# Performance work log

Hardware: AMD Instinct MI355X
Metric: run time of the kernel (lower is better)

## Reference

```python
import jax, jax.numpy as jnp
import numpy as np

N, E, D, F, H = 20000, 600000, 128, 128, 4
C = 2 * D + F  # concat(source, sink, edge) feature dim


def _ln(x, g, b, eps=1e-5):
    mu = jnp.mean(x, -1, keepdims=True)
    v = jnp.mean((x - mu) ** 2, -1, keepdims=True)
    return (x - mu) / jnp.sqrt(v + eps) * g + b


def _gelu(x):
    return jax.nn.gelu(x, approximate=False)  # torch default exact GELU


def setup_inputs() -> dict:
    key = jax.random.key(0)
    ks = iter(jax.random.split(key, 40))

    def nrm(shape, s=0.05):
        return jax.random.normal(next(ks), shape, dtype=jnp.float32) * s

    inp = {}
    inp["bb_nodes"] = jax.random.normal(next(ks), (N, D), dtype=jnp.float32)
    inp["eattr"] = jax.random.normal(next(ks), (E, F), dtype=jnp.float32)
    inp["eidx"] = jax.random.randint(next(ks), (2, E), 0, N)
    inp["aW_w"] = nrm((H, D, C)); inp["aW_b"] = nrm((H, D))
    inp["aA_w"] = nrm((H, D));    inp["aA_b"] = nrm((H,))
    inp["nw1"] = nrm((D, C)); inp["nb1"] = nrm((D,))
    inp["nw2"] = nrm((D, D)); inp["nb2"] = nrm((D,))
    inp["nw3"] = nrm((D, D)); inp["nb3"] = nrm((D,))
    inp["dw1"] = nrm((4 * D, D)); inp["db1"] = nrm((4 * D,))
    inp["dw2"] = nrm((D, 4 * D)); inp["db2"] = nrm((D,))
    inp["ew1"] = nrm((F, C)); inp["eb1"] = nrm((F,))
    inp["ew2"] = nrm((F, F)); inp["eb2"] = nrm((F,))
    inp["ew3"] = nrm((F, F)); inp["eb3"] = nrm((F,))
    inp["aggr_w"] = nrm((D, H * D)); inp["aggr_b"] = nrm((D,))
    inp["ln1_g"] = jnp.ones((D,), jnp.float32); inp["ln1_b"] = jnp.zeros((D,), jnp.float32)
    inp["lne_g"] = jnp.ones((F,), jnp.float32); inp["lne_b"] = jnp.zeros((F,), jnp.float32)
    return inp


def reference(bb_nodes, eattr, eidx, aW_w, aW_b, aA_w, aA_b,
              nw1, nb1, nw2, nb2, nw3, nb3,
              dw1, db1, dw2, db2,
              ew1, eb1, ew2, eb2, ew3, eb3,
              aggr_w, aggr_b, ln1_g, ln1_b, lne_g, lne_b):
    n = bb_nodes.shape[0]
    src, snk = eidx[0], eidx[1]
    h = jnp.concatenate([bb_nodes[src], bb_nodes[snk], eattr], axis=1)  # [E, 2D+F]
    nheads = aW_w.shape[0]
    # per-head GAT-style logits; loop over small fixed head count to keep
    # peak memory at [E, D] per head rather than [H, E, D]
    logits = jnp.stack(
        [jax.nn.leaky_relu(h @ aW_w[k].T + aW_b[k], 0.2) @ aA_w[k] + aA_b[k]
         for k in range(nheads)], axis=1)                              # [E, H]
    msg = _gelu(h @ nw1.T + nb1)
    msg = _gelu(msg @ nw2.T + nb2)
    msg = msg @ nw3.T + nb3                                            # [E, D]
    # segment softmax over incoming edges of each sink node
    smax = jax.ops.segment_max(logits, snk, num_segments=n)            # [N, H]
    att = jnp.exp(logits - smax[snk])                                  # [E, H]
    norm = jax.ops.segment_sum(att + 1e-12, snk, num_segments=n)       # [N, H]
    att = att / norm[snk]
    # NOTE: faithful to the original's `atten[:, eidx[1]]` which re-gathers
    # the per-EDGE attention along the edge axis using NODE indices.
    att_g = att[snk]                                                   # [E, H]
    agg = jnp.stack(
        [jax.ops.segment_sum(att_g[:, k, None] * msg, snk, num_segments=n)
         for k in range(nheads)], axis=1)                              # [N, H, D]
    upd = agg.reshape(n, -1) @ aggr_w.T + aggr_b                       # [N, D]
    x = _ln(bb_nodes + upd, ln1_g, ln1_b)
    dense = _gelu(x @ dw1.T + db1) @ dw2.T + db2
    # original adds the attention update (not x) in the second residual,
    # and reuses node_norm1 both times (node_norm2 is dead code)
    x = _ln(dense + upd, ln1_g, ln1_b)
    eu = jnp.concatenate([x[src], x[snk], eattr], axis=1)              # [E, 2D+F]
    eu = _gelu(eu @ ew1.T + eb1)
    eu = _gelu(eu @ ew2.T + eb2)
    eu = eu @ ew3.T + eb3
    eout = _ln(eattr + eu, lne_g, lne_b)
    return x, eout
```

## Files before the change

### kernel.cpp

```cpp
#include <hip/hip_runtime.h>
#include <hip/hip_bf16.h>

#define N_NODES 20000
#define N_EDGES 600000
#define HEADS 4
#define MAXDEG 128

#define WOFF_AW   0
#define WOFF_NW1  196608
#define WOFF_NW2  245760
#define WOFF_NW3  262144
#define WOFF_EW1  278528
#define WOFF_EW2  327680
#define WOFF_EW3  344064
#define WOFF_AG   360448
#define WOFF_DW1  425984
#define WOFF_DW2  491520
#define WPACK_TOT 557056

typedef __attribute__((ext_vector_type(8))) short s16x8;
typedef __attribute__((ext_vector_type(4))) float f32x4;
typedef unsigned int u32;
typedef unsigned short u16;

__device__ __forceinline__ float bf2f(u16 h){ return __uint_as_float(((u32)h)<<16); }
__device__ __forceinline__ u16 f2bf(float f){
  u32 u = __float_as_uint(f) + 0x8000u;
  return (u16)(u>>16);
}
__device__ __forceinline__ float gelu_f(float x){
  float z2 = 1.5957691216057308f*(x + 0.044715f*x*x*x);
  float e = __expf(z2);
  float th = 1.f - 2.f/(e + 1.f);
  return 0.5f*x*(1.f + th);
}

__device__ __forceinline__ int swzf(int row){ return (row&15)<<4; }

__global__ __launch_bounds__(256) void k_pack(
    const float* __restrict__ aW, const float* __restrict__ nw1, const float* __restrict__ nw2,
    const float* __restrict__ nw3, const float* __restrict__ ew1, const float* __restrict__ ew2,
    const float* __restrict__ ew3, const float* __restrict__ aggr_w, const float* __restrict__ dw1,
    const float* __restrict__ dw2, const float* __restrict__ bb,
    u16* __restrict__ wpk, u16* __restrict__ bbp)
{
  int i = blockIdx.x*256 + threadIdx.x;
  if (i < WPACK_TOT){
    const float* src; int rel; int KROW;
    if      (i < WOFF_NW1){ src=aW;     rel=i;           KROW=384; }
    else if (i < WOFF_NW2){ src=nw1;    rel=i-WOFF_NW1;  KROW=384; }
    else if (i < WOFF_NW3){ src=nw2;    rel=i-WOFF_NW2;  KROW=128; }
    else if (i < WOFF_EW1){ src=nw3;    rel=i-WOFF_NW3;  KROW=128; }
    else if (i < WOFF_EW2){ src=ew1;    rel=i-WOFF_EW1;  KROW=384; }
    else if (i < WOFF_EW3){ src=ew2;    rel=i-WOFF_EW2;  KROW=128; }
    else if (i < WOFF_AG) { src=ew3;    rel=i-WOFF_EW3;  KROW=128; }
    else if (i < WOFF_DW1){ src=aggr_w; rel=i-WOFF_AG;   KROW=512; }
    else if (i < WOFF_DW2){ src=dw1;    rel=i-WOFF_DW1;  KROW=128; }
    else                  { src=dw2;    rel=i-WOFF_DW2;  KROW=512; }
    int e = rel&7, lane = (rel>>3)&63, frag = rel>>9;
    int ks, g;
    if      (KROW==384){ ks = frag % 12; g = frag / 12; }
    else if (KROW==128){ ks = frag & 3;  g = frag >> 2; }
    else               { ks = frag & 15; g = frag >> 4; }
    int row = g*16 + (lane&15);
    int k   = ks*32 + ((lane>>4)&3)*8 + e;
    wpk[i] = f2bf(src[(size_t)row*KROW + k]);
  }
  if (i < N_NODES*128) bbp[i] = f2bf(bb[i]);
}

__global__ __launch_bounds__(256) void k_init(float* __restrict__ norm, u32* __restrict__ cnt)
{
  int i = blockIdx.x*256 + threadIdx.x;
  if (i < N_NODES*HEADS) norm[i] = 0.f;
  if (i < N_NODES) cnt[i] = 0u;
}

template<int NT, int KS, int RS>
__device__ __forceinline__ void gemmF(const char* ab, const u16* __restrict__ wfrag,
                                      int g0, int l, f32x4 (&acc)[4][NT])
{
  const int l15 = l&15, lg = l>>4;
  const int swz = l15<<4;
  const u16* wl = wfrag + l*8;
  #pragma unroll 4
  for (int ks=0; ks<KS; ++ks){
    s16x8 af[4];
    #pragma unroll
    for (int mt=0;mt<4;++mt)
      af[mt] = *(const s16x8*)(ab + (mt*16+l15)*RS + (((ks*4+lg)*16) ^ swz));
    #pragma unroll
    for (int nt=0;nt<NT;++nt){
      s16x8 bf = *(const s16x8*)(wl + (size_t)((g0+nt)*KS + ks)*512);
      #pragma unroll
      for (int mt=0;mt<4;++mt)
        acc[mt][nt] = __builtin_amdgcn_mfma_f32_16x16x32_bf16(af[mt], bf, acc[mt][nt], 0,0,0);
    }
  }
}

template<int KSI, int RS, int KSTOT>
__device__ __forceinline__ void gemmF2(const char* ab, const u16* __restrict__ wfrag,
                                       int g0, int ks0, int l, f32x4 (&acc)[4][1])
{
  const int l15 = l&15, lg = l>>4;
  const int swz = l15<<4;
  const u16* wl = wfrag + l*8;
  #pragma unroll 4
  for (int ks=0; ks<KSI; ++ks){
    s16x8 af[4];
    #pragma unroll
    for (int mt=0;mt<4;++mt)
      af[mt] = *(const s16x8*)(ab + (mt*16+l15)*RS + (((ks*4+lg)*16) ^ swz));
    s16x8 bf = *(const s16x8*)(wl + (size_t)(g0*KSTOT + ks0 + ks)*512);
    #pragma unroll
    for (int mt=0;mt<4;++mt)
      acc[mt][0] = __builtin_amdgcn_mfma_f32_16x16x32_bf16(af[mt], bf, acc[mt][0], 0,0,0);
  }
}

template<int RS>
__device__ __forceinline__ void writeReg(char* hsb, int regionByte, int col, int lg,
                                         const float (&v)[4][4])
{
  #pragma unroll
  for (int mt=0;mt<4;++mt){
    #pragma unroll
    for (int r=0;r<4;++r){
      int row = mt*16 + lg*4 + r;
      *(u16*)(hsb + row*RS + regionByte + ((col*2) ^ swzf(row))) = f2bf(v[mt][r]);
    }
  }
}

__device__ __forceinline__ void stage512(char* hsb, const u16* __restrict__ ntab,
                                         const float* __restrict__ eattr, const int* __restrict__ eidx,
                                         int e0, int t)
{
  const int row = t>>3, p = t&7, ge = e0+row;
  const int swz = swzf(row);
  char* rp = hsb + row*768;
  if (p < 4){
    int nid = eidx[(p<2 ? 0 : N_EDGES) + ge];
    const int4* srow = (const int4*)(ntab + (size_t)nid*128);
    const int base = (p<2) ? 0 : 16;
    #pragma unroll
    for (int s=0;s<8;++s){
      int ci = (2*s + p) & 15;
      int4 v = srow[ci];
      *(int4*)(rp + (((base+ci)*16) ^ swz)) = v;
    }
  } else {
    int q = p-4;
    const float* er = eattr + (size_t)ge*128 + q*32;
    #pragma unroll
    for (int c=0;c<4;++c){
      float4 x0 = ((const float4*)er)[c*2];
      float4 x1 = ((const float4*)er)[c*2+1];
      int4 v;
      v.x = (int)((u32)f2bf(x0.x) | ((u32)f2bf(x0.y)<<16));
      v.y = (int)((u32)f2bf(x0.z) | ((u32)f2bf(x0.w)<<16));
      v.z = (int)((u32)f2bf(x1.x) | ((u32)f2bf(x1.y)<<16));
      v.w = (int)((u32)f2bf(x1.z) | ((u32)f2bf(x1.w)<<16));
      *(int4*)(rp + (((32 + q*4 + c)*16) ^ swz)) = v;
    }
  }
}

__global__ __launch_bounds__(512,4) void k_edgeA(
  const u16* __restrict__ bbp, const float* __restrict__ eattr, const int* __restrict__ eidx,
  const u16* __restrict__ wpk,
  const float* __restrict__ aW_b, const float* __restrict__ aA_w, const float* __restrict__ aA_b,
  const float* __restrict__ nb1, const float* __restrict__ nb2, const float* __restrict__ nb3,
  float* __restrict__ logits, float* __restrict__ norm, u32* __restrict__ cnt,
  int* __restrict__ eids2, u16* __restrict__ msg)
{
  __shared__ u16 hs[64*384];
  __shared__ float lpart[8*64];
  __shared__ int snkid[64];
  char* hsb = (char*)hs;
  const int t = threadIdx.x;
  const int e0 = blockIdx.x*64;
  const int w = t>>6, l = t&63, l15 = l&15, lg = l>>4;
  const int col = w*16 + l15;

  stage512(hsb, bbp, eattr, eidx, e0, t);
  lpart[w*64 + l] = 0.f;
  if (t < 64){
    int k = eidx[N_EDGES + e0 + t];
    snkid[t] = k;
    u32 pos = atomicAdd(&cnt[k], 1u);
    if (pos < MAXDEG) eids2[k*MAXDEG + pos] = e0 + t;
  }
  __syncthreads();

  {
    #pragma unroll
    for (int ch=0; ch<2; ++ch){
      f32x4 acc[4][2];
      #pragma unroll
      for (int mt=0;mt<4;++mt){
        #pragma unroll
        for (int nt=0;nt<2;++nt){ f32x4 z={0.f,0.f,0.f,0.f}; acc[mt][nt]=z; }
      }
      int g0 = (w>>1)*8 + (w&1)*4 + ch*2;
      gemmF<2,12,768>(hsb, wpk+WOFF_AW, g0, l, acc);
      float lp[4][4];
      #pragma unroll
      for (int a=0;a<4;++a){
        #pragma unroll
        for (int b=0;b<4;++b) lp[a][b]=0.f;
      }
      #pragma unroll
      for (int nt=0;nt<2;++nt){
        int gcol = (w>>1)*128 + (w&1)*64 + ch*32 + nt*16 + l15;
        float bia = aW_b[gcol];
        float avw = aA_w[gcol];
        #pragma unroll
        for (int mt=0;mt<4;++mt){
          #pragma unroll
          for (int r=0;r<4;++r){
            float T = acc[mt][nt][r] + bia;
            T = (T>0.f) ? T : 0.2f*T;
            lp[mt][r] += T*avw;
          }
        }
      }
      #pragma unroll
      for (int mt=0;mt<4;++mt){
        #pragma unroll
        for (int r=0;r<4;++r){
          float v = lp[mt][r];
          v += __shfl_xor(v,1);
          v += __shfl_xor(v,2);
          v += __shfl_xor(v,4);
          v += __shfl_xor(v,8);
          if (l15==0) lpart[w*64 + mt*16 + lg*4 + r] += v;
        }
      }
    }
  }
  float m1v[4][4];
  {
    f32x4 acc[4][1];
    #pragma unroll
    for (int mt=0;mt<4;++mt){ f32x4 z={0.f,0.f,0.f,0.f}; acc[mt][0]=z; }
    gemmF<1,12,768>(hsb, wpk+WOFF_NW1, w, l, acc);
    float b = nb1[col];
    #pragma unroll
    for (int mt=0;mt<4;++mt){
      #pragma unroll
      for (int r=0;r<4;++r) m1v[mt][r] = gelu_f(acc[mt][0][r] + b);
    }
  }
  __syncthreads();

  if (t < 256){
    int row = t>>2, h = t&3;
    float s = lpart[(2*h)*64 + row] + lpart[(2*h+1)*64 + row] + aA_b[h];
    int e = e0 + row;
    logits[e*HEADS + h] = s;
    atomicAdd(&norm[snkid[row]*HEADS + h], expf(s));
  }
  writeReg<768>(hsb, 0, col, lg, m1v);
  __syncthreads();

  {
    f32x4 acc[4][1];
    #pragma unroll
    for (int mt=0;mt<4;++mt){ f32x4 z={0.f,0.f,0.f,0.f}; acc[mt][0]=z; }
    gemmF<1,4,768>(hsb, wpk+WOFF_NW2, w, l, acc);
    float b = nb2[col];
    float v[4][4];
    #pragma unroll
    for (int mt=0;mt<4;++mt){
      #pragma unroll
      for (int r=0;r<4;++r) v[mt][r] = gelu_f(acc[mt][0][r] + b);
    }
    writeReg<768>(hsb, 256, col, lg, v);
  }
  __syncthreads();

  {
    f32x4 acc[4][1];
    #pragma unroll
    for (int mt=0;mt<4;++mt){ f32x4 z={0.f,0.f,0.f,0.f}; acc[mt][0]=z; }
    gemmF<1,4,768>(hsb+256, wpk+WOFF_NW3, w, l, acc);
    float b = nb3[col];
    float v[4][4];
    #pragma unroll
    for (int mt=0;mt<4;++mt){
      #pragma unroll
      for (int r=0;r<4;++r) v[mt][r] = acc[mt][0][r] + b;
    }
    writeReg<768>(hsb, 512, col, lg, v);
  }
  __syncthreads();

  {
    int row = t>>3, p = t&7;
    const int swz = swzf(row);
    #pragma unroll
    for (int c=0;c<2;++c){
      int j = c*8 + p;
      int4 v = *(const int4*)(hsb + row*768 + 512 + ((j*16) ^ swz));
      *(int4*)((char*)msg + (size_t)(e0+row)*256 + j*16) = v;
    }
  }
}

__global__ __launch_bounds__(256) void k_msgsumZ(
  const u16* __restrict__ msg, const int* __restrict__ eids2, const u32* __restrict__ cnt,
  const int* __restrict__ eidx, const float* __restrict__ logits,
  const float* __restrict__ norm,
  u16* __restrict__ z)
{
  __shared__ float red[4][128];
  __shared__ float av[4];
  const int n = blockIdx.x, t = threadIdx.x;
  u32* zrow = (u32*)z + (size_t)n*256;
  if (n >= N_NODES){
    zrow[t] = 0u;
    return;
  }
  const int w = t>>6, l = t&63;
  int ecnt = (int)cnt[n]; if (ecnt > MAXDEG) ecnt = MAXDEG;
  float a0=0.f, a1=0.f;
  for (int i=w; i<ecnt; i+=4){
    int e = eids2[n*MAXDEG + i];
    u32 v = *(const u32*)(msg + (size_t)e*128 + l*2);
    a0 += __uint_as_float(v<<16);
    a1 += __uint_as_float(v & 0xFFFF0000u);
  }
  red[w][l*2] = a0; red[w][l*2+1] = a1;
  if (t < 4){
    int sn = eidx[N_EDGES + n];
    float c = 1e-12f * (float)cnt[sn];
    av[t] = expf(logits[n*HEADS+t]) / (norm[sn*HEADS+t] + c);
  }
  __syncthreads();
  int h = t>>6, dp = (t&63)*2;
  float s0 = red[0][dp]+red[1][dp]+red[2][dp]+red[3][dp];
  float s1 = red[0][dp+1]+red[1][dp+1]+red[2][dp+1]+red[3][dp+1];
  float a = av[h];
  zrow[h*64 + (t&63)] = (u32)f2bf(a*s0) | ((u32)f2bf(a*s1)<<16);
}

__global__ __launch_bounds__(512,2) void k_node(
  const u16* __restrict__ z, const float* __restrict__ bb,
  const u16* __restrict__ wpk, const float* __restrict__ aggr_b,
  const float* __restrict__ db1, const float* __restrict__ db2,
  const float* __restrict__ lng, const float* __restrict__ lnb,
  float* __restrict__ xout, u16* __restrict__ xbp)
{
  __shared__ u16 hs[64*512];
  __shared__ float lps[8*64];
  __shared__ float lpss[8*64];
  __shared__ float mrs[2*64];
  char* hsb = (char*)hs;
  const int t = threadIdx.x;
  const int nbase = blockIdx.x*64;
  const int w = t>>6, l = t&63, l15 = l&15, lg = l>>4;
  const int col = w*16 + l15;

  {
    const int row = t>>3, p = t&7;
    const int swz = swzf(row);
    char* rp = hsb + row*1024;
    const int4* zr = (const int4*)((const char*)z + (size_t)(nbase+row)*1024);
    #pragma unroll
    for (int c=0;c<8;++c){
      int ci = c*8 + p;
      int4 v = zr[ci];
      *(int4*)(rp + ((ci*16) ^ swz)) = v;
    }
  }
  __syncthreads();

  float v[4][4];
  {
    f32x4 acc[4][1];
    #pragma unroll
    for (int mt=0;mt<4;++mt){ f32x4 z_={0.f,0.f,0.f,0.f}; acc[mt][0]=z_; }
    gemmF<1,16,1024>(hsb, wpk+WOFF_AG, w, l, acc);
    float ab = aggr_b[col];
    #pragma unroll
    for (int mt=0;mt<4;++mt){
      #pragma unroll
      for (int r=0;r<4;++r) v[mt][r] = acc[mt][0][r] + ab;
    }
  }
  __syncthreads();

  {
    float xv[4][4];
    #pragma unroll
    for (int mt=0;mt<4;++mt){
      #pragma unroll
      for (int r=0;r<4;++r){
        int row = mt*16 + lg*4 + r;
        int ge = nbase + row; if (ge >= N_NODES) ge = N_NODES-1;
        xv[mt][r] = bb[(size_t)ge*128 + col] + v[mt][r];
      }
    }
    #pragma unroll
    for (int mt=0;mt<4;++mt){
      #pragma unroll
      for (int r=0;r<4;++r){
        float a = xv[mt][r], b = xv[mt][r]*xv[mt][r];
        a += __shfl_xor(a,1); b += __shfl_xor(b,1);
        a += __shfl_xor(a,2); b += __shfl_xor(b,2);
        a += __shfl_xor(a,4); b += __shfl_xor(b,4);
        a += __shfl_xor(a,8); b += __shfl_xor(b,8);
        if (l15==0){
          int row = mt*16 + lg*4 + r;
          lps[w*64 + row] = a;
          lpss[w*64 + row] = b;
        }
      }
    }
    __syncthreads();
    if (t < 64){
      float a=0.f, b=0.f;
      #pragma unroll
      for (int j=0;j<8;++j){ a += lps[j*64+t]; b += lpss[j*64+t]; }
      float mu = a*(1.f/128.f);
      float var = b*(1.f/128.f) - mu*mu;
      mrs[t] = mu;
      mrs[64+t] = rsqrtf(var + 1e-5f);
    }
    __syncthreads();
    float g = lng[col], bt = lnb[col];
    float xb[4][4];
    #pragma unroll
    for (int mt=0;mt<4;++mt){
      #pragma unroll
      for (int r=0;r<4;++r){
        int row = mt*16 + lg*4 + r;
        xb[mt][r] = (xv[mt][r] - mrs[row])*mrs[64+row]*g + bt;
      }
    }
    writeReg<1024>(hsb, 0, col, lg, xb);
  }
  __syncthreads();

  f32x4 acc3[4][1];
  #pragma unroll
  for (int mt=0;mt<4;++mt){ f32x4 z_={0.f,0.f,0.f,0.f}; acc3[mt][0]=z_; }
  #pragma unroll
  for (int c=0;c<4;++c){
    {
      f32x4 acc[4][1];
      #pragma unroll
      for (int mt=0;mt<4;++mt){ f32x4 z_={0.f,0.f,0.f,0.f}; acc[mt][0]=z_; }
      gemmF<1,4,1024>(hsb, wpk+WOFF_DW1, c*8 + w, l, acc);
      float b1 = db1[c*128 + col];
      float dh[4][4];
      #pragma unroll
      for (int mt=0;mt<4;++mt){
        #pragma unroll
        for (int r=0;r<4;++r) dh[mt][r] = gelu_f(acc[mt][0][r] + b1);
      }
      writeReg<1024>(hsb, 256 + (c&1)*256, col, lg, dh);
    }
    __syncthreads();
    gemmF2<4,1024,16>(hsb + 256 + (c&1)*256, wpk+WOFF_DW2, w, c*4, l, acc3);
  }

  {
    float ov[4][4];
    float b2 = db2[col];
    #pragma unroll
    for (int mt=0;mt<4;++mt){
      #pragma unroll
      for (int r=0;r<4;++r) ov[mt][r] = acc3[mt][0][r] + b2 + v[mt][r];
    }
    #pragma unroll
    for (int mt=0;mt<4;++mt){
      #pragma unroll
      for (int r=0;r<4;++r){
        float a = ov[mt][r], b = ov[mt][r]*ov[mt][r];
        a += __shfl_xor(a,1); b += __shfl_xor(b,1);
        a += __shfl_xor(a,2); b += __shfl_xor(b,2);
        a += __shfl_xor(a,4); b += __shfl_xor(b,4);
        a += __shfl_xor(a,8); b += __shfl_xor(b,8);
        if (l15==0){
          int row = mt*16 + lg*4 + r;
          lps[w*64 + row] = a;
          lpss[w*64 + row] = b;
        }
      }
    }
    __syncthreads();
    if (t < 64){
      float a=0.f, b=0.f;
      #pragma unroll
      for (int j=0;j<8;++j){ a += lps[j*64+t]; b += lpss[j*64+t]; }
      float mu = a*(1.f/128.f);
      float var = b*(1.f/128.f) - mu*mu;
      mrs[t] = mu;
      mrs[64+t] = rsqrtf(var + 1e-5f);
    }
    __syncthreads();
    float g = lng[col], bt = lnb[col];
    #pragma unroll
    for (int mt=0;mt<4;++mt){
      #pragma unroll
      for (int r=0;r<4;++r){
        int row = mt*16 + lg*4 + r;
        int ge = nbase + row;
        if (ge < N_NODES){
          float o = (ov[mt][r] - mrs[row])*mrs[64+row]*g + bt;
          xout[(size_t)ge*128 + col] = o;
          xbp[(size_t)ge*128 + col] = f2bf(o);
        }
      }
    }
  }
}

__global__ __launch_bounds__(512,4) void k_edgeC(
  const u16* __restrict__ xbp, const float* __restrict__ eattr, const int* __restrict__ eidx,
  const u16* __restrict__ wpk,
  const float* __restrict__ eb1, const float* __restrict__ eb2, const float* __restrict__ eb3,
  const float* __restrict__ lng, const float* __restrict__ lnb,
  float* __restrict__ eout)
{
  __shared__ u16 hs[64*384];
  __shared__ float wps[8*64];
  __shared__ float wpss[8*64];
  __shared__ float mrs[2*64];
  char* hsb=(char*)hs;
  const int t = threadIdx.x;
  const int e0 = blockIdx.x*64;
  const int w = t>>6, l = t&63, l15 = l&15, lg = l>>4;
  const int col = w*16 + l15;

  stage512(hsb, xbp, eattr, eidx, e0, t);
  __syncthreads();

  float e1v[4][4];
  {
    f32x4 acc[4][1];
    #pragma unroll
    for (int mt=0;mt<4;++mt){ f32x4 z={0.f,0.f,0.f,0.f}; acc[mt][0]=z; }
    gemmF<1,12,768>(hsb, wpk+WOFF_EW1, w, l, acc);
    float b = eb1[col];
    #pragma unroll
    for (int mt=0;mt<4;++mt){
      #pragma unroll
      for (int r=0;r<4;++r) e1v[mt][r] = gelu_f(acc[mt][0][r] + b);
    }
  }
  __syncthreads();
  writeReg<768>(hsb, 0, col, lg, e1v);
  __syncthreads();

  {
    f32x4 acc[4][1];
    #pragma unroll
    for (int mt=0;mt<4;++mt){ f32x4 z={0.f,0.f,0.f,0.f}; acc[mt][0]=z; }
    gemmF<1,4,768>(hsb, wpk+WOFF_EW2, w, l, acc);
    float b = eb2[col];
    float v[4][4];
    #pragma unroll
    for (int mt=0;mt<4;++mt){
      #pragma unroll
      for (int r=0;r<4;++r) v[mt][r] = gelu_f(acc[mt][0][r] + b);
    }
    writeReg<768>(hsb, 256, col, lg, v);
  }
  __syncthreads();

  {
    f32x4 acc[4][1];
    #pragma unroll
    for (int mt=0;mt<4;++mt){ f32x4 z={0.f,0.f,0.f,0.f}; acc[mt][0]=z; }
    gemmF<1,4,768>(hsb+256, wpk+WOFF_EW3, w, l, acc);
    float b3 = eb3[col];
    float v[4][4];
    #pragma unroll
    for (int mt=0;mt<4;++mt){
      #pragma unroll
      for (int r=0;r<4;++r){
        int row = mt*16 + lg*4 + r;
        float ea = bf2f(*(const u16*)(hsb + row*768 + 512 + ((col*2) ^ swzf(row))));
        v[mt][r] = acc[mt][0][r] + b3 + ea;
      }
    }
    #pragma unroll
    for (int mt=0;mt<4;++mt){
      #pragma unroll
      for (int r=0;r<4;++r){
        float a = v[mt][r], b = v[mt][r]*v[mt][r];
        a += __shfl_xor(a,1); b += __shfl_xor(b,1);
        a += __shfl_xor(a,2); b += __shfl_xor(b,2);
        a += __shfl_xor(a,4); b += __shfl_xor(b,4);
        a += __shfl_xor(a,8); b += __shfl_xor(b,8);
        if (l15==0){
          int row = mt*16 + lg*4 + r;
          wps[w*64 + row] = a;
          wpss[w*64 + row] = b;
        }
      }
    }
    __syncthreads();
    if (t < 64){
      float a=0.f, b=0.f;
      #pragma unroll
      for (int j=0;j<8;++j){ a += wps[j*64+t]; b += wpss[j*64+t]; }
      float mu = a*(1.f/128.f);
      float var = b*(1.f/128.f) - mu*mu;
      mrs[t] = mu;
      mrs[64+t] = rsqrtf(var + 1e-5f);
    }
    __syncthreads();
    float g = lng[col], bb_ = lnb[col];
    #pragma unroll
    for (int mt=0;mt<4;++mt){
      #pragma unroll
      for (int r=0;r<4;++r){
        int row = mt*16 + lg*4 + r;
        float o = (v[mt][r] - mrs[row])*mrs[64+row]*g + bb_;
        eout[(size_t)(e0+row)*128 + col] = o;
      }
    }
  }
}

static inline size_t alup(size_t x){ return (x + 255) & ~(size_t)255; }

extern "C" void kernel_launch(void* const* d_in, const int* in_sizes, int n_in,
                              void* d_out, int out_size, void* d_ws, size_t ws_size,
                              hipStream_t stream)
{
  (void)in_sizes; (void)n_in; (void)out_size; (void)ws_size;
  const float* bb    = (const float*)d_in[0];
  const float* eattr = (const float*)d_in[1];
  const int*   eidx  = (const int*)d_in[2];
  const float* aW_w  = (const float*)d_in[3];
  const float* aW_b  = (const float*)d_in[4];
  const float* aA_w  = (const float*)d_in[5];
  const float* aA_b  = (const float*)d_in[6];
  const float* nw1   = (const float*)d_in[7];
  const float* nb1   = (const float*)d_in[8];
  const float* nw2   = (const float*)d_in[9];
  const float* nb2   = (const float*)d_in[10];
  const float* nw3   = (const float*)d_in[11];
  const float* nb3   = (const float*)d_in[12];
  const float* dw1   = (const float*)d_in[13];
  const float* db1   = (const float*)d_in[14];
  const float* dw2   = (const float*)d_in[15];
  const float* db2   = (const float*)d_in[16];
  const float* ew1   = (const float*)d_in[17];
  const float* eb1   = (const float*)d_in[18];
  const float* ew2   = (const float*)d_in[19];
  const float* eb2   = (const float*)d_in[20];
  const float* ew3   = (const float*)d_in[21];
  const float* eb3   = (const float*)d_in[22];
  const float* aggr_w= (const float*)d_in[23];
  const float* aggr_b= (const float*)d_in[24];
  const float* ln1g  = (const float*)d_in[25];
  const float* ln1b  = (const float*)d_in[26];
  const float* lneg  = (const float*)d_in[27];
  const float* lneb  = (const float*)d_in[28];

  char* p = (char*)d_ws;
  auto take = [&](size_t bytes)->char*{ char* r = p; p += alup(bytes); return r; };
  u16*   wpk    = (u16*)  take((size_t)WPACK_TOT*2);
  u16*   bbp    = (u16*)  take((size_t)N_NODES*128*2);
  u16*   xbp    = (u16*)  take((size_t)N_NODES*128*2);
  float* logits = (float*)take((size_t)N_EDGES*HEADS*4);
  float* norm   = (float*)take((size_t)N_NODES*HEADS*4);
  u32*   cnt    = (u32*)  take((size_t)N_NODES*4);
  int*   eids2  = (int*)  take((size_t)N_NODES*MAXDEG*4);
  u16*   z      = (u16*)  take((size_t)20032*512*2);

  float* xout = (float*)d_out;
  float* eout = xout + (size_t)N_NODES*128;
  u16*   msg  = (u16*)eout;

  k_pack    <<<dim3(10000), dim3(256), 0, stream>>>(aW_w,nw1,nw2,nw3,ew1,ew2,ew3,aggr_w,dw1,dw2,bb,wpk,bbp);
  k_init    <<<dim3(313),   dim3(256), 0, stream>>>(norm,cnt);
  k_edgeA   <<<dim3(9375),  dim3(512), 0, stream>>>(bbp,eattr,eidx,wpk,aW_b,aA_w,aA_b,nb1,nb2,nb3,logits,norm,cnt,eids2,msg);
  k_msgsumZ <<<dim3(20032), dim3(256), 0, stream>>>(msg,eids2,cnt,eidx,logits,norm,z);
  k_node    <<<dim3(313),   dim3(512), 0, stream>>>(z,bb,wpk,aggr_b,db1,db2,ln1g,ln1b,xout,xbp);
  k_edgeC   <<<dim3(9375),  dim3(512), 0, stream>>>(xbp,eattr,eidx,wpk,eb1,eb2,eb3,lneg,lneb,eout);
}
```

Baseline: 1.061 ms.

## Stage edge tiles in MFMA fragment-interleaved LDS layout and skip unused logit writes

Replaces the row-major swizzled shared-memory tile with a layout arranged per MFMA A-fragment, used everywhere in k_edgeA. Global staging, the intermediate writebacks and the final msg readout all use the new layout, and a new GEMM helper reads whole A fragments with one load each. The aim is cheaper, conflict-free LDS reads in the GEMM inner loops, at the cost of scalar 2-byte writebacks between stages. It also writes logits only for edges whose index is below the node count, since the later re-gather reads only those rows, and computes leaky ReLU with fmaxf.

```diff
diff --git a/kernel.cpp b/kernel.cpp
--- a/kernel.cpp
+++ b/kernel.cpp
@@ -167,6 +167,42 @@
   }
 }
 
+template<int NT, int KS, int KSB>
+__device__ __forceinline__ void gemmFI(const char* abase, const u16* __restrict__ wfrag,
+                                       int g0, int l, f32x4 (&acc)[4][NT])
+{
+  const u16* wl = wfrag + (size_t)g0*KS*512 + l*8;
+  #pragma unroll 4
+  for (int ks=0; ks<KS; ++ks){
+    const char* ap = abase + (size_t)(KSB+ks)*1024;
+    s16x8 af[4];
+    #pragma unroll
+    for (int mt=0;mt<4;++mt)
+      af[mt] = *(const s16x8*)(ap + mt*12288);
+    #pragma unroll
+    for (int nt=0;nt<NT;++nt){
+      s16x8 bf = *(const s16x8*)(wl + (size_t)(nt*KS + ks)*512);
+      #pragma unroll
+      for (int mt=0;mt<4;++mt)
+        acc[mt][nt] = __builtin_amdgcn_mfma_f32_16x16x32_bf16(af[mt], bf, acc[mt][nt], 0,0,0);
+    }
+  }
+}
+
+__device__ __forceinline__ void writeFragA(char* hsb, int ksBase, int w, int l15, int lg,
+                                           const float (&v)[4][4])
+{
+  int lg2 = ((w&1)<<1) + (l15>>3);
+  int b0 = (ksBase + (w>>1))*1024 + lg2*256 + lg*64 + (lg2<<4) + (l15&7)*2;
+  #pragma unroll
+  for (int r=0;r<4;++r){
+    int off = b0 ^ (r<<4);
+    #pragma unroll
+    for (int mt=0;mt<4;++mt)
+      *(u16*)(hsb + off + mt*12288) = f2bf(v[mt][r]);
+  }
+}
+
 __global__ __launch_bounds__(512,4) void k_edgeA(
   const u16* __restrict__ bbp, const float* __restrict__ eattr, const int* __restrict__ eidx,
   const u16* __restrict__ wpk,
@@ -183,8 +219,31 @@
   const int e0 = blockIdx.x*64;
   const int w = t>>6, l = t&63, l15 = l&15, lg = l>>4;
   const int col = w*16 + l15;
-
-  stage512(hsb, bbp, eattr, eidx, e0, t);
+  const char* abase = hsb + lg*256 + ((l15 ^ lg)<<4);
+
+  {
+    #pragma unroll
+    for (int i=0;i<6;++i){
+      int B = w*6 + i;
+      int m = B/12, ks = B - m*12;
+      int row = m*16 + l15;
+      char* dst = hsb + B*1024 + lg*256 + ((l15 ^ lg)<<4);
+      if (ks < 8){
+        int nid = eidx[(ks<4 ? 0 : N_EDGES) + e0 + row];
+        *(int4*)dst = *(const int4*)(bbp + (size_t)nid*128 + (ks&3)*32 + lg*8);
+      } else {
+        const float* er = eattr + (size_t)(e0+row)*128 + (ks&3)*32 + lg*8;
+        float4 x0 = ((const float4*)er)[0];
+        float4 x1 = ((const float4*)er)[1];
+        int4 v;
+        v.x = (int)((u32)f2bf(x0.x) | ((u32)f2bf(x0.y)<<16));
+        v.y = (int)((u32)f2bf(x0.z) | ((u32)f2bf(x0.w)<<16));
+        v.z = (int)((u32)f2bf(x1.x) | ((u32)f2bf(x1.y)<<16));
+        v.w = (int)((u32)f2bf(x1.z) | ((u32)f2bf(x1.w)<<16));
+        *(int4*)dst = v;
+      }
+    }
+  }
   lpart[w*64 + l] = 0.f;
   if (t < 64){
     int k = eidx[N_EDGES + e0 + t];
@@ -204,7 +263,7 @@
         for (int nt=0;nt<2;++nt){ f32x4 z={0.f,0.f,0.f,0.f}; acc[mt][nt]=z; }
       }
       int g0 = (w>>1)*8 + (w&1)*4 + ch*2;
-      gemmF<2,12,768>(hsb, wpk+WOFF_AW, g0, l, acc);
+      gemmFI<2,12,0>(abase, wpk+WOFF_AW, g0, l, acc);
       float lp[4][4];
       #pragma unroll
       for (int a=0;a<4;++a){
@@ -221,7 +280,7 @@
           #pragma unroll
           for (int r=0;r<4;++r){
             float T = acc[mt][nt][r] + bia;
-            T = (T>0.f) ? T : 0.2f*T;
+            T = fmaxf(T, 0.2f*T);
             lp[mt][r] += T*avw;
           }
         }
@@ -245,7 +304,7 @@
     f32x4 acc[4][1];
     #pragma unroll
     for (int mt=0;mt<4;++mt){ f32x4 z={0.f,0.f,0.f,0.f}; acc[mt][0]=z; }
-    gemmF<1,12,768>(hsb, wpk+WOFF_NW1, w, l, acc);
+    gemmFI<1,12,0>(abase, wpk+WOFF_NW1, w, l, acc);
     float b = nb1[col];
     #pragma unroll
     for (int mt=0;mt<4;++mt){
@@ -259,17 +318,17 @@
     int row = t>>2, h = t&3;
     float s = lpart[(2*h)*64 + row] + lpart[(2*h+1)*64 + row] + aA_b[h];
     int e = e0 + row;
-    logits[e*HEADS + h] = s;
+    if (e0 < N_NODES) logits[e*HEADS + h] = s;
     atomicAdd(&norm[snkid[row]*HEADS + h], expf(s));
   }
-  writeReg<768>(hsb, 0, col, lg, m1v);
+  writeFragA(hsb, 0, w, l15, lg, m1v);
   __syncthreads();
 
   {
     f32x4 acc[4][1];
     #pragma unroll
     for (int mt=0;mt<4;++mt){ f32x4 z={0.f,0.f,0.f,0.f}; acc[mt][0]=z; }
-    gemmF<1,4,768>(hsb, wpk+WOFF_NW2, w, l, acc);
+    gemmFI<1,4,0>(abase, wpk+WOFF_NW2, w, l, acc);
     float b = nb2[col];
     float v[4][4];
     #pragma unroll
@@ -277,7 +336,7 @@
       #pragma unroll
       for (int r=0;r<4;++r) v[mt][r] = gelu_f(acc[mt][0][r] + b);
     }
-    writeReg<768>(hsb, 256, col, lg, v);
+    writeFragA(hsb, 4, w, l15, lg, v);
   }
   __syncthreads();
 
@@ -285,7 +344,7 @@
     f32x4 acc[4][1];
     #pragma unroll
     for (int mt=0;mt<4;++mt){ f32x4 z={0.f,0.f,0.f,0.f}; acc[mt][0]=z; }
-    gemmF<1,4,768>(hsb+256, wpk+WOFF_NW3, w, l, acc);
+    gemmFI<1,4,4>(abase, wpk+WOFF_NW3, w, l, acc);
     float b = nb3[col];
     float v[4][4];
     #pragma unroll
@@ -293,17 +352,18 @@
       #pragma unroll
       for (int r=0;r<4;++r) v[mt][r] = acc[mt][0][r] + b;
     }
-    writeReg<768>(hsb, 512, col, lg, v);
+    writeFragA(hsb, 8, w, l15, lg, v);
   }
   __syncthreads();
 
   {
     int row = t>>3, p = t&7;
-    const int swz = swzf(row);
+    int mb = (row>>4)*12 + 8;
     #pragma unroll
     for (int c=0;c<2;++c){
       int j = c*8 + p;
-      int4 v = *(const int4*)(hsb + row*768 + 512 + ((j*16) ^ swz));
+      int off = (mb + (j>>2))*1024 + (j&3)*256 + (((row&15) ^ (j&3))<<4);
+      int4 v = *(const int4*)(hsb + off);
       *(int4*)((char*)msg + (size_t)(e0+row)*256 + j*16) = v;
     }
   }
```

New measurement: 1.142 ms. 1.08x slower.
